# Performance work log

Measured on AMD Instinct MI355X. Metric: run time of the kernel, lower is better.

## Reference

```python
import jax, jax.numpy as jnp
import numpy as np

SIGMA_COLOR = 0.1
SIGMA_SPATIAL = 5.0
RADIUS = 8


def setup_inputs() -> dict:
    key = jax.random.key(0)
    images = jax.random.uniform(key, (16, 3, 768, 768), dtype=jnp.float32)
    return {"images": images}


def _spatial_affinity(h, w):
    # coordinates of each cell in the (h, w) feature grid, flattened to N = h*w
    y = jnp.repeat(jnp.arange(h, dtype=jnp.float32), w)  # [N]
    x = jnp.tile(jnp.arange(w, dtype=jnp.float32), h)    # [N]
    y_diff = y[:, None] - y[None, :]                      # [N, N]
    x_diff = x[:, None] - x[None, :]                      # [N, N]
    spatial_dist = y_diff ** 2 + x_diff ** 2
    aff = jnp.exp(-spatial_dist / (2.0 * SIGMA_SPATIAL ** 2))
    mask = (jnp.abs(y_diff) <= RADIUS) & (jnp.abs(x_diff) <= RADIUS)
    return aff * mask.astype(aff.dtype)                   # [N, N]


def reference(images):
    B, C, H, W = images.shape
    h, w = H // 16, W // 16
    N = h * w
    # bilinear resize, half-pixel centers == torch align_corners=False
    img_r = jax.image.resize(images, (B, C, h, w), method="bilinear", antialias=False)
    feats = img_r.reshape(B, C, N).transpose(0, 2, 1)     # [B, N, C]
    # ||f_i - f_j||^2 = |f_i|^2 + |f_j|^2 - 2 f_i . f_j  (avoids [B,N,N,C] diff tensor)
    sq = jnp.sum(feats * feats, axis=-1)                  # [B, N]
    dots = jnp.einsum("bic,bjc->bij", feats, feats)       # [B, N, N]
    color_dist = jnp.maximum(sq[:, :, None] + sq[:, None, :] - 2.0 * dots, 0.0)
    color_aff = jnp.exp(-color_dist / (2.0 * SIGMA_COLOR ** 2))  # [B, N, N]
    spatial_aff = _spatial_affinity(h, w)                 # [N, N]
    return color_aff * spatial_aff[None, :, :]            # [B, N, N]
```

## Files before the change

kernel.cpp:

```cpp
#include <hip/hip_runtime.h>

#define BATCH 16
#define CH    3
#define HIN   768
#define WIN   768
#define HS    48
#define WS    48
#define NPIX  (HS * WS)
#define QPR   (NPIX / 4)
#define ROWS_PB 4

typedef float f32x4 __attribute__((ext_vector_type(4)));

__global__ void downsample_kernel(const float* __restrict__ img,
                                  f32x4* __restrict__ feats) {
    int idx = blockIdx.x * blockDim.x + threadIdx.x;
    if (idx >= BATCH * NPIX) return;
    int b = idx / NPIX;
    int n = idx - b * NPIX;
    int y = n / WS;
    int x = n - y * WS;
    int iy = 16 * y + 7;
    int ix = 16 * x + 7;
    const float* base = img + (size_t)b * CH * HIN * WIN;
    float f[3];
#pragma unroll
    for (int c = 0; c < 3; ++c) {
        const float* p = base + (size_t)c * HIN * WIN;
        const float* r0 = p + (size_t)iy * WIN + ix;
        const float* r1 = r0 + WIN;
        f[c] = 0.25f * (r0[0] + r0[1] + r1[0] + r1[1]);
    }
    f32x4 v = {f[0], f[1], f[2], 0.0f};
    feats[idx] = v;
}

__global__ __launch_bounds__(256) void affinity_kernel(const f32x4* __restrict__ feats,
                                                       f32x4* __restrict__ out) {
    const int tid = threadIdx.x;
    const int b   = blockIdx.y;
    const int i0  = blockIdx.x * ROWS_PB;
    const f32x4* __restrict__ frow = feats + b * NPIX;

#pragma unroll
    for (int ii = 0; ii < ROWS_PB; ++ii) {
        const int i  = i0 + ii;
        const int yi = i / WS;
        const int xi = i - yi * WS;
        const f32x4 fi = frow[i];
        f32x4* __restrict__ orow = out + (size_t)(b * NPIX + i) * QPR;

#pragma unroll
        for (int qi = 0; qi < 3; ++qi) {
            const int q = tid + qi * 256;
            if (qi < 2 || q < QPR) {
                const int yj  = q / 12;
                const int xj0 = (q - yj * 12) * 4;
                const int dy  = yi - yj;
                f32x4 r = {0.f, 0.f, 0.f, 0.f};
                if ((unsigned)(dy + 8) <= 16u) {
                    const float sdy = (float)(dy * dy);
#pragma unroll
                    for (int k = 0; k < 4; ++k) {
                        const int dx = xi - (xj0 + k);
                        const f32x4 fj = frow[4 * q + k];
                        const float d0 = fi.x - fj.x;
                        const float d1 = fi.y - fj.y;
                        const float d2 = fi.z - fj.z;
                        const float cd = d0 * d0 + d1 * d1 + d2 * d2;
                        const float sd = sdy + (float)(dx * dx);
                        const float e  = __expf(-50.0f * cd - 0.02f * sd);
                        r[k] = ((unsigned)(dx + 8) <= 16u) ? e : 0.0f;
                    }
                }
                __builtin_nontemporal_store(r, &orow[q]);
            }
        }
    }
}

extern "C" void kernel_launch(void* const* d_in, const int* in_sizes, int n_in,
                              void* d_out, int out_size, void* d_ws, size_t ws_size,
                              hipStream_t stream) {
    const float* img = (const float*)d_in[0];
    f32x4* feats = (f32x4*)d_ws;
    f32x4* out   = (f32x4*)d_out;

    {
        int threads = BATCH * NPIX;
        int block = 256;
        int grid = (threads + block - 1) / block;
        downsample_kernel<<<grid, block, 0, stream>>>(img, feats);
    }
    {
        dim3 grid(NPIX / ROWS_PB, BATCH);
        affinity_kernel<<<grid, 256, 0, stream>>>(feats, out);
    }
}
```

Measured before the change: 394.8 us.

## Compute only the spatial band per row block and bulk-zero the rest

Restricts exp and feature loads to the band of columns within the spatial radius shared by the block's four rows, loading neighbor features once per thread and reusing them across rows. Columns outside the band are written as zeros by the other threads. This removes redundant loads and masked computation but drops the nontemporal store hint and changes the store pattern per thread.

```diff
diff --git a/kernel.cpp b/kernel.cpp
--- a/kernel.cpp
+++ b/kernel.cpp
@@ -40,41 +40,66 @@
     const int tid = threadIdx.x;
     const int b   = blockIdx.y;
     const int i0  = blockIdx.x * ROWS_PB;
-    const f32x4* __restrict__ frow = feats + b * NPIX;
+    const int yi  = i0 / WS;
+    const int xi0 = i0 - yi * WS;
 
+    const int ylo   = (yi - 8 > 0) ? yi - 8 : 0;
+    const int yhi   = (yi + 8 < HS - 1) ? yi + 8 : HS - 1;
+    const int qlo   = 12 * ylo;
+    const int qhi   = 12 * (yhi + 1);
+    const int bandw = qhi - qlo;
+    const int nz    = QPR - bandw;
+
+    const f32x4* __restrict__ frow  = feats + b * NPIX;
+    f32x4* __restrict__       obase = out + (size_t)(b * NPIX + i0) * QPR;
+
+    const bool inband = tid < bandw;
+    int   q = 0, xj[4];
+    float sdy = 0.0f;
+    f32x4 fj[4];
+    if (inband) {
+        q = qlo + tid;
+        const int yj  = q / 12;
+        const int dy  = yi - yj;
+        sdy = (float)(dy * dy);
+        const int xj0 = (q - yj * 12) * 4;
 #pragma unroll
-    for (int ii = 0; ii < ROWS_PB; ++ii) {
-        const int i  = i0 + ii;
-        const int yi = i / WS;
-        const int xi = i - yi * WS;
-        const f32x4 fi = frow[i];
-        f32x4* __restrict__ orow = out + (size_t)(b * NPIX + i) * QPR;
+        for (int k = 0; k < 4; ++k) {
+            xj[k] = xj0 + k;
+            fj[k] = frow[4 * q + k];
+        }
+    }
 
+    const f32x4 z = {0.f, 0.f, 0.f, 0.f};
 #pragma unroll
-        for (int qi = 0; qi < 3; ++qi) {
-            const int q = tid + qi * 256;
-            if (qi < 2 || q < QPR) {
-                const int yj  = q / 12;
-                const int xj0 = (q - yj * 12) * 4;
-                const int dy  = yi - yj;
-                f32x4 r = {0.f, 0.f, 0.f, 0.f};
-                if ((unsigned)(dy + 8) <= 16u) {
-                    const float sdy = (float)(dy * dy);
+    for (int iter = 0; iter < 2; ++iter) {
+        const int t2 = tid + 256 * iter;
+        if (t2 < nz) {
+            const int zq = (t2 < qlo) ? t2 : t2 + bandw;
 #pragma unroll
-                    for (int k = 0; k < 4; ++k) {
-                        const int dx = xi - (xj0 + k);
-                        const f32x4 fj = frow[4 * q + k];
-                        const float d0 = fi.x - fj.x;
-                        const float d1 = fi.y - fj.y;
-                        const float d2 = fi.z - fj.z;
-                        const float cd = d0 * d0 + d1 * d1 + d2 * d2;
-                        const float sd = sdy + (float)(dx * dx);
-                        const float e  = __expf(-50.0f * cd - 0.02f * sd);
-                        r[k] = ((unsigned)(dx + 8) <= 16u) ? e : 0.0f;
-                    }
-                }
-                __builtin_nontemporal_store(r, &orow[q]);
+            for (int ii = 0; ii < ROWS_PB; ++ii)
+                obase[(size_t)ii * QPR + zq] = z;
+        }
+    }
+
+    if (inband) {
+#pragma unroll
+        for (int ii = 0; ii < ROWS_PB; ++ii) {
+            const f32x4 fi = frow[i0 + ii];
+            const int   xi = xi0 + ii;
+            f32x4 r;
+#pragma unroll
+            for (int k = 0; k < 4; ++k) {
+                const int   dx = xi - xj[k];
+                const float d0 = fi.x - fj[k].x;
+                const float d1 = fi.y - fj[k].y;
+                const float d2 = fi.z - fj[k].z;
+                const float cd = d0 * d0 + d1 * d1 + d2 * d2;
+                const float sd = sdy + (float)(dx * dx);
+                const float e  = __expf(-50.0f * cd - 0.02f * sd);
+                r[k] = ((unsigned)(dx + 8) <= 16u) ? e : 0.0f;
             }
+            obase[(size_t)ii * QPR + q] = r;
         }
     }
 }
```

Result: no change. 391.1 us (-0.9%).

## Process one spatial row per block with j-features kept in registers

Applied to the files above, without the earlier changes.

Each block now handles an entire image row of 48 query pixels. The neighbour features for each thread's output column are loaded once into registers and reused across all rows, and thread-to-column slot selection is restricted to the valid vertical band. This removes repeated feature loads and index arithmetic per row. In exchange the grid shrinks to far fewer blocks, and nontemporal stores become regular stores, which may reduce memory-level parallelism and cache behaviour for the large output write.

```diff
diff --git a/kernel.cpp b/kernel.cpp
--- a/kernel.cpp
+++ b/kernel.cpp
@@ -8,7 +8,6 @@
 #define WS    48
 #define NPIX  (HS * WS)
 #define QPR   (NPIX / 4)
-#define ROWS_PB 4
 
 typedef float f32x4 __attribute__((ext_vector_type(4)));
 
@@ -38,42 +37,62 @@
 __global__ __launch_bounds__(256) void affinity_kernel(const f32x4* __restrict__ feats,
                                                        f32x4* __restrict__ out) {
     const int tid = threadIdx.x;
+    const int yi  = blockIdx.x;
     const int b   = blockIdx.y;
-    const int i0  = blockIdx.x * ROWS_PB;
-    const f32x4* __restrict__ frow = feats + b * NPIX;
+    const int i0  = yi * WS;
 
+    const f32x4* __restrict__ frow  = feats + b * NPIX;
+    f32x4* __restrict__       obase = out + (size_t)(b * NPIX + i0) * QPR;
+
+    const int ylo = (yi - 8 > 0) ? yi - 8 : 0;
+    const int yhi = (yi + 8 < HS - 1) ? yi + 8 : HS - 1;
+    const int qlo = 12 * ylo;
+    const int qhi = 12 * (yhi + 1);
+
+    int slot = -1, xj0 = 0;
+    float sdy = 0.0f;
+    f32x4 fj0 = {0,0,0,0}, fj1 = {0,0,0,0}, fj2 = {0,0,0,0}, fj3 = {0,0,0,0};
 #pragma unroll
-    for (int ii = 0; ii < ROWS_PB; ++ii) {
-        const int i  = i0 + ii;
-        const int yi = i / WS;
-        const int xi = i - yi * WS;
-        const f32x4 fi = frow[i];
-        f32x4* __restrict__ orow = out + (size_t)(b * NPIX + i) * QPR;
+    for (int s = 0; s < 3; ++s) {
+        const int q = tid + 256 * s;
+        if (q < QPR && q >= qlo && q < qhi) slot = s;
+    }
+    if (slot >= 0) {
+        const int q  = tid + 256 * slot;
+        const int yj = q / 12;
+        const int dy = yi - yj;
+        sdy = (float)(dy * dy);
+        xj0 = (q - yj * 12) * 4;
+        fj0 = frow[4 * q + 0];
+        fj1 = frow[4 * q + 1];
+        fj2 = frow[4 * q + 2];
+        fj3 = frow[4 * q + 3];
+    }
 
+    const f32x4 z = {0.f, 0.f, 0.f, 0.f};
+#pragma unroll 1
+    for (int ii = 0; ii < WS; ++ii) {
+        const f32x4 fi = frow[i0 + ii];
+        f32x4* __restrict__ orow = obase + (size_t)ii * QPR;
 #pragma unroll
-        for (int qi = 0; qi < 3; ++qi) {
-            const int q = tid + qi * 256;
-            if (qi < 2 || q < QPR) {
-                const int yj  = q / 12;
-                const int xj0 = (q - yj * 12) * 4;
-                const int dy  = yi - yj;
-                f32x4 r = {0.f, 0.f, 0.f, 0.f};
-                if ((unsigned)(dy + 8) <= 16u) {
-                    const float sdy = (float)(dy * dy);
+        for (int s = 0; s < 3; ++s) {
+            if (s < 2 || tid < QPR - 512) {
+                f32x4 r = z;
+                if (s == slot) {
+                    const f32x4 fjv[4] = {fj0, fj1, fj2, fj3};
 #pragma unroll
                     for (int k = 0; k < 4; ++k) {
-                        const int dx = xi - (xj0 + k);
-                        const f32x4 fj = frow[4 * q + k];
-                        const float d0 = fi.x - fj.x;
-                        const float d1 = fi.y - fj.y;
-                        const float d2 = fi.z - fj.z;
+                        const int   dx = ii - (xj0 + k);
+                        const float d0 = fi.x - fjv[k].x;
+                        const float d1 = fi.y - fjv[k].y;
+                        const float d2 = fi.z - fjv[k].z;
                         const float cd = d0 * d0 + d1 * d1 + d2 * d2;
                         const float sd = sdy + (float)(dx * dx);
                         const float e  = __expf(-50.0f * cd - 0.02f * sd);
                         r[k] = ((unsigned)(dx + 8) <= 16u) ? e : 0.0f;
                     }
                 }
-                __builtin_nontemporal_store(r, &orow[q]);
+                orow[tid + 256 * s] = r;
             }
         }
     }
@@ -93,7 +112,7 @@
         downsample_kernel<<<grid, block, 0, stream>>>(img, feats);
     }
     {
-        dim3 grid(NPIX / ROWS_PB, BATCH);
+        dim3 grid(HS, BATCH);
         affinity_kernel<<<grid, 256, 0, stream>>>(feats, out);
     }
 }
```

After: 395.4 us. About the same (+0.1%).
